# Optimization experiments

Hardware: AMD Instinct MI355X
Metric: run time of the kernel (lower is better)

The kernel has to match this reference:

```python
import jax, jax.numpy as jnp
import numpy as np

EMBED = 1024
HEADS = 16
HEAD_DIM = EMBED // HEADS


def setup_inputs() -> dict:
    key = jax.random.key(0)
    ks = jax.random.split(key, 11)
    B, S, E = 4, 2048, EMBED
    scale = 1.0 / np.sqrt(E)
    inp = {
        "Q": jax.random.normal(ks[0], (B, S, E), jnp.float32),
        "K": jax.random.normal(ks[1], (B, S, E), jnp.float32),
        "V": jax.random.normal(ks[2], (B, S, E), jnp.float32),
        "Wq": jax.random.normal(ks[3], (E, E), jnp.float32) * scale,
        "Wk": jax.random.normal(ks[4], (E, E), jnp.float32) * scale,
        "Wv": jax.random.normal(ks[5], (E, E), jnp.float32) * scale,
        "Wo": jax.random.normal(ks[6], (E, E), jnp.float32) * scale,
        "bq": jax.random.normal(ks[7], (E,), jnp.float32) * 0.01,
        "bk": jax.random.normal(ks[8], (E,), jnp.float32) * 0.01,
        "bv": jax.random.normal(ks[9], (E,), jnp.float32) * 0.01,
        "bo": jax.random.normal(ks[10], (E,), jnp.float32) * 0.01,
    }
    return inp


def reference(Q, K, V, Wq, Wk, Wv, Wo, bq, bk, bv, bo):
    B, S, E = Q.shape
    H, Dh = HEADS, HEAD_DIM
    # linear projections (torch Linear: x @ W.T + b)
    q = (Q @ Wq.T + bq).reshape(B, S, H, Dh).transpose(0, 2, 1, 3)  # [B,H,S,Dh]
    k = (K @ Wk.T + bk).reshape(B, S, H, Dh).transpose(0, 2, 1, 3)
    v = (V @ Wv.T + bv).reshape(B, S, H, Dh).transpose(0, 2, 1, 3)
    # scores [B,H,S,S]
    A = jnp.einsum('bhqd,bhkd->bhqk', q, k) / np.sqrt(Dh).astype(np.float32)
    # causal mask (mask=True)
    causal = jnp.tril(jnp.ones((S, S), dtype=bool))
    A = jnp.where(causal, A, -jnp.inf)
    w = jax.nn.softmax(A, axis=-1)
    out = jnp.einsum('bhqk,bhkd->bhqd', w, v)  # [B,H,S,Dh]
    out = out.transpose(0, 2, 1, 3).reshape(B, S, E)
    return out @ Wo.T + bo
```

## Files before the change

### kernel.cpp

```cpp
#include <hip/hip_runtime.h>
#include <hip/hip_bf16.h>
#include <hip/hip_fp16.h>

#define E_DIM 1024
#define N_HEADS 16
#define DH 64
#define BATCH 4
#define SEQ 2048
#define MROWS (BATCH * SEQ)
#define NQT 16

using half8 = __attribute__((ext_vector_type(8))) _Float16;
using half4v = __attribute__((ext_vector_type(4))) _Float16;
using fp16x2 = __attribute__((ext_vector_type(2))) __fp16;
using f32x4 = __attribute__((ext_vector_type(4))) float;

#define LOG2E 1.44269504088896340736f

__device__ inline half8 ld8(const _Float16* p) { return *(const half8*)p; }

__device__ inline uint32_t lds_off(const void* p) {
    return (uint32_t)(uintptr_t)(const __attribute__((address_space(3))) char*)p;
}

__device__ inline float exp2fast(float x) {
    float r;
    asm("v_exp_f32 %0, %1" : "=v"(r) : "v"(x));
    return r;
}

__global__ void cast3_f16(const float* __restrict__ a0, const float* __restrict__ a1,
                          const float* __restrict__ a2,
                          _Float16* __restrict__ o0, _Float16* __restrict__ o1,
                          _Float16* __restrict__ o2, int n4) {
    const int z = blockIdx.y;
    const float* in = z == 0 ? a0 : z == 1 ? a1 : a2;
    _Float16* out = z == 0 ? o0 : z == 1 ? o1 : o2;
    int i = blockIdx.x * blockDim.x + threadIdx.x;
    if (i < n4) {
        float4 v = *(const float4*)(in + (size_t)i * 4);
        half4v o;
        o[0] = (_Float16)v.x; o[1] = (_Float16)v.y;
        o[2] = (_Float16)v.z; o[3] = (_Float16)v.w;
        *(half4v*)(out + (size_t)i * 4) = o;
    }
}
__global__ void cast4_f16(const float* __restrict__ a0, const float* __restrict__ a1,
                          const float* __restrict__ a2, const float* __restrict__ a3,
                          _Float16* __restrict__ o0, _Float16* __restrict__ o1,
                          _Float16* __restrict__ o2, _Float16* __restrict__ o3, int n4) {
    const int z = blockIdx.y;
    const float* in = z == 0 ? a0 : z == 1 ? a1 : z == 2 ? a2 : a3;
    _Float16* out = z == 0 ? o0 : z == 1 ? o1 : z == 2 ? o2 : o3;
    int i = blockIdx.x * blockDim.x + threadIdx.x;
    if (i < n4) {
        float4 v = *(const float4*)(in + (size_t)i * 4);
        half4v o;
        o[0] = (_Float16)v.x; o[1] = (_Float16)v.y;
        o[2] = (_Float16)v.z; o[3] = (_Float16)v.w;
        *(half4v*)(out + (size_t)i * 4) = o;
    }
}

template <int MODE>
__device__ __forceinline__ void gemm_body(
    const _Float16* __restrict__ A, const _Float16* __restrict__ Bt,
    const float* __restrict__ bias, void* __restrict__ outp,
    int N, int K, float scale, _Float16* As, _Float16* Bs)
{
    const int t = threadIdx.x;
    const int w = t >> 6, l = t & 63;
    const int wr = w >> 1, wc = w & 1;
    const int lr = l & 15, lg = l >> 4;
    const long row0 = (long)blockIdx.x * 128;
    const long col0 = (long)blockIdx.y * 128;
    f32x4 acc[4][4] = {};

    for (int k0 = 0; k0 < K; k0 += 32) {
        __syncthreads();
        #pragma unroll
        for (int p = 0; p < 2; ++p) {
            const int n = p * 256 + t;
            const int row = n >> 2, c8 = (n & 3) << 3;
            const _Float16* ga = &A[(size_t)(row0 + row) * K + k0 + c8];
            const _Float16* gb = &Bt[(size_t)(col0 + row) * K + k0 + c8];
            __builtin_amdgcn_global_load_lds(
                (const __attribute__((address_space(1))) unsigned int*)ga,
                (__attribute__((address_space(3))) unsigned int*)((char*)As + n * 16), 16, 0, 0);
            __builtin_amdgcn_global_load_lds(
                (const __attribute__((address_space(1))) unsigned int*)gb,
                (__attribute__((address_space(3))) unsigned int*)((char*)Bs + n * 16), 16, 0, 0);
        }
        __syncthreads();
        half8 af[4], bf[4];
        #pragma unroll
        for (int i = 0; i < 4; i++) {
            af[i] = *(const half8*)&As[(wr * 64 + i * 16 + lr) * 32 + lg * 8];
            bf[i] = *(const half8*)&Bs[(wc * 64 + i * 16 + lr) * 32 + lg * 8];
        }
        #pragma unroll
        for (int i = 0; i < 4; i++)
            #pragma unroll
            for (int j = 0; j < 4; j++)
                acc[i][j] = __builtin_amdgcn_mfma_f32_16x16x32_f16(af[i], bf[j], acc[i][j], 0, 0, 0);
    }

    #pragma unroll
    for (int i = 0; i < 4; i++)
        #pragma unroll
        for (int j = 0; j < 4; j++)
            #pragma unroll
            for (int r = 0; r < 4; r++) {
                long row = row0 + wr * 64 + i * 16 + lg * 4 + r;
                long col = col0 + wc * 64 + j * 16 + lr;
                float v = acc[i][j][r] + bias[col];
                if (MODE == 0) {
                    ((float*)outp)[row * N + col] = v;
                } else {
                    long b = row >> 11, s = row & 2047;
                    long h = col >> 6, d = col & 63;
                    ((_Float16*)outp)[(((b * N_HEADS + h) * SEQ + s) << 6) + d] =
                        (_Float16)(v * scale);
                }
            }
}

__global__ __launch_bounds__(256) void gemm_qkv(
    const _Float16* __restrict__ A0, const _Float16* __restrict__ A1,
    const _Float16* __restrict__ A2,
    const _Float16* __restrict__ W0, const _Float16* __restrict__ W1,
    const _Float16* __restrict__ W2,
    const float* __restrict__ b0, const float* __restrict__ b1,
    const float* __restrict__ b2,
    _Float16* __restrict__ o0, _Float16* __restrict__ o1, _Float16* __restrict__ o2)
{
    __shared__ _Float16 As[128 * 32];
    __shared__ _Float16 Bs[128 * 32];
    const int z = blockIdx.z;
    const _Float16* A = z == 0 ? A0 : z == 1 ? A1 : A2;
    const _Float16* W = z == 0 ? W0 : z == 1 ? W1 : W2;
    const float* bia = z == 0 ? b0 : z == 1 ? b1 : b2;
    _Float16* o = z == 0 ? o0 : z == 1 ? o1 : o2;
    const float scale = z == 0 ? (0.125f * LOG2E) : 1.0f;
    gemm_body<1>(A, W, bia, o, E_DIM, E_DIM, scale, As, Bs);
}

__global__ __launch_bounds__(256) void gemm_out(
    const _Float16* __restrict__ A, const _Float16* __restrict__ W,
    const float* __restrict__ bias, float* __restrict__ o)
{
    __shared__ _Float16 As[128 * 32];
    __shared__ _Float16 Bs[128 * 32];
    gemm_body<0>(A, W, bias, o, E_DIM, E_DIM, 1.0f, As, Bs);
}

__global__ __launch_bounds__(256) void attn_fwd(
    const _Float16* __restrict__ qb, const _Float16* __restrict__ kb,
    const _Float16* __restrict__ vb, _Float16* __restrict__ ob)
{
    __shared__ _Float16 sB[3 * 8192];
    const int bh = blockIdx.x;
    const int tile = (NQT - 1) - blockIdx.y;
    const int t = threadIdx.x;
    const int w = t >> 6, l = t & 63;
    const int lr = l & 15, lg = l >> 4;
    const _Float16* qh = qb + (size_t)bh * SEQ * DH;
    const char* khc = (const char*)(kb + (size_t)bh * SEQ * DH);
    const char* vhc = (const char*)(vb + (size_t)bh * SEQ * DH);
    char* sBc = (char*)sB;
    const uint32_t ldsbase = lds_off(sB);
    const int b = bh >> 4, h = bh & 15;

    int koff[2], voff[2];
    #pragma unroll
    for (int i = 0; i < 2; ++i) {
        const int s = i * 256 + t;
        { const int r = s >> 3, c = (s & 7) ^ (r & 7);
          koff[i] = r * 128 + c * 16; }
        { const int r = ((s >> 5) << 2) | ((s >> 1) & 3);
          const int c = (((s >> 3) & 3) << 1) | (s & 1);
          voff[i] = r * 128 + c * 16; }
    }

    const int nt = 2 * tile + 2;
    const int q0 = tile * 128 + w * 16;
    const int q1 = q0 + 64;

    half8 qf00 = ld8(&qh[(q0 + lr) * DH + lg * 8]);
    half8 qf01 = ld8(&qh[(q0 + lr) * DH + 32 + lg * 8]);
    half8 qf10 = ld8(&qh[(q1 + lr) * DH + lg * 8]);
    half8 qf11 = ld8(&qh[(q1 + lr) * DH + 32 + lg * 8]);

    #define STAGE(TI, BUF) do {                                                   \
        const char* ks_ = khc + (size_t)(TI) * 8192;                              \
        const char* vs_ = vhc + (size_t)(TI) * 8192;                              \
        char* kd_ = sBc + (BUF) * 16384;                                          \
        char* vd_ = kd_ + 8192;                                                   \
        _Pragma("unroll")                                                         \
        for (int i_ = 0; i_ < 2; ++i_) {                                          \
            __builtin_amdgcn_global_load_lds(                                     \
                (const __attribute__((address_space(1))) unsigned int*)(ks_ + koff[i_]), \
                (__attribute__((address_space(3))) unsigned int*)(kd_ + i_ * 4096 + t * 16), 16, 0, 0); \
            __builtin_amdgcn_global_load_lds(                                     \
                (const __attribute__((address_space(1))) unsigned int*)(vs_ + voff[i_]), \
                (__attribute__((address_space(3))) unsigned int*)(vd_ + i_ * 4096 + t * 16), 16, 0, 0); \
        }                                                                         \
    } while (0)

    STAGE(0, 0);
    STAGE(1, 1);

    f32x4 acc0[4] = {}, acc1[4] = {};
    float m0 = -1e30f, l0 = 0.f, m1 = -1e30f, l1 = 0.f;

    int cur = 0;
    #pragma unroll 1
    for (int it = 0; it < nt; ++it) {
        if (it + 1 < nt) asm volatile("s_waitcnt vmcnt(4)" ::: "memory");
        else             asm volatile("s_waitcnt vmcnt(0)" ::: "memory");
        __builtin_amdgcn_s_barrier();
        if (it + 2 < nt) {
            int nb = cur + 2; if (nb >= 3) nb -= 3;
            STAGE(it + 2, nb);
        }

        const char* kbuf = sBc + cur * 16384;
        const uint32_t vbuf = ldsbase + (uint32_t)cur * 16384u + 8192u;
        const bool a0 = (it <= 2 * tile);
        const bool diag0 = (it == 2 * tile);
        const bool diag1 = (it == 2 * tile + 1);

        f32x4 st0[4], st1[4];
        __builtin_amdgcn_s_setprio(1);
        #pragma unroll
        for (int sub = 0; sub < 4; ++sub) {
            const int row = sub * 16 + lr;
            half8 kf0 = *(const half8*)(kbuf + ((row * 128 + lg * 16) ^ ((row & 7) << 4)));
            half8 kf1 = *(const half8*)(kbuf + ((row * 128 + 64 + lg * 16) ^ ((row & 7) << 4)));
            f32x4 s1 = {};
            s1 = __builtin_amdgcn_mfma_f32_16x16x32_f16(kf0, qf10, s1, 0, 0, 0);
            s1 = __builtin_amdgcn_mfma_f32_16x16x32_f16(kf1, qf11, s1, 0, 0, 0);
            st1[sub] = s1;
            if (a0) {
                f32x4 s0 = {};
                s0 = __builtin_amdgcn_mfma_f32_16x16x32_f16(kf0, qf00, s0, 0, 0, 0);
                s0 = __builtin_amdgcn_mfma_f32_16x16x32_f16(kf1, qf01, s0, 0, 0, 0);
                st0[sub] = s0;
            }
        }
        __builtin_amdgcn_s_setprio(0);

        half4v pa0[4], pa1[4];

        if (a0) {
            if (diag0) {
                #pragma unroll
                for (int sub = 0; sub < 4; ++sub)
                    #pragma unroll
                    for (int r = 0; r < 4; ++r)
                        if (sub * 16 + lg * 4 + r > w * 16 + lr) st0[sub][r] = -1e30f;
            }
            float a = fmaxf(fmaxf(st0[0][0], st0[0][1]), st0[0][2]);
            float bb = fmaxf(fmaxf(st0[0][3], st0[1][0]), st0[1][1]);
            float c = fmaxf(fmaxf(st0[1][2], st0[1][3]), st0[2][0]);
            float d = fmaxf(fmaxf(st0[2][1], st0[2][2]), st0[2][3]);
            float e = fmaxf(fmaxf(st0[3][0], st0[3][1]), st0[3][2]);
            float tmax = fmaxf(fmaxf(fmaxf(a, bb), fmaxf(c, d)), fmaxf(e, st0[3][3]));
            tmax = fmaxf(tmax, __shfl_xor(tmax, 16, 64));
            tmax = fmaxf(tmax, __shfl_xor(tmax, 32, 64));
            const bool skip = __all(tmax <= m0 + 10.0f);
            float fscale = 1.0f;
            if (!skip) { const float mn = fmaxf(m0, tmax); fscale = exp2fast(m0 - mn); m0 = mn; }
            float psum = 0.f;
            fp16x2 ones; ones[0] = (__fp16)1.f; ones[1] = (__fp16)1.f;
            #pragma unroll
            for (int sub = 0; sub < 4; ++sub) {
                float pv[4];
                #pragma unroll
                for (int r = 0; r < 4; ++r) pv[r] = exp2fast(st0[sub][r] - m0);
                fp16x2 lo = __builtin_amdgcn_cvt_pkrtz(pv[0], pv[1]);
                fp16x2 hi = __builtin_amdgcn_cvt_pkrtz(pv[2], pv[3]);
                psum = __builtin_amdgcn_fdot2(lo, ones, psum, false);
                psum = __builtin_amdgcn_fdot2(hi, ones, psum, false);
                pa0[sub][0] = (_Float16)lo[0]; pa0[sub][1] = (_Float16)lo[1];
                pa0[sub][2] = (_Float16)hi[0]; pa0[sub][3] = (_Float16)hi[1];
            }
            l0 = l0 * fscale + psum;
            if (!skip) {
                #pragma unroll
                for (int r = 0; r < 4; ++r) {
                    const float fr = __shfl(fscale, lg * 4 + r, 64);
                    acc0[0][r] *= fr; acc0[1][r] *= fr; acc0[2][r] *= fr; acc0[3][r] *= fr;
                }
            }
        }

        {
            if (diag1) {
                #pragma unroll
                for (int sub = 0; sub < 4; ++sub)
                    #pragma unroll
                    for (int r = 0; r < 4; ++r)
                        if (sub * 16 + lg * 4 + r > w * 16 + lr) st1[sub][r] = -1e30f;
            }
            float a = fmaxf(fmaxf(st1[0][0], st1[0][1]), st1[0][2]);
            float bb = fmaxf(fmaxf(st1[0][3], st1[1][0]), st1[1][1]);
            float c = fmaxf(fmaxf(st1[1][2], st1[1][3]), st1[2][0]);
            float d = fmaxf(fmaxf(st1[2][1], st1[2][2]), st1[2][3]);
            float e = fmaxf(fmaxf(st1[3][0], st1[3][1]), st1[3][2]);
            float tmax = fmaxf(fmaxf(fmaxf(a, bb), fmaxf(c, d)), fmaxf(e, st1[3][3]));
            tmax = fmaxf(tmax, __shfl_xor(tmax, 16, 64));
            tmax = fmaxf(tmax, __shfl_xor(tmax, 32, 64));
            const bool skip = __all(tmax <= m1 + 10.0f);
            float fscale = 1.0f;
            if (!skip) { const float mn = fmaxf(m1, tmax); fscale = exp2fast(m1 - mn); m1 = mn; }
            float psum = 0.f;
            fp16x2 ones; ones[0] = (__fp16)1.f; ones[1] = (__fp16)1.f;
            #pragma unroll
            for (int sub = 0; sub < 4; ++sub) {
                float pv[4];
                #pragma unroll
                for (int r = 0; r < 4; ++r) pv[r] = exp2fast(st1[sub][r] - m1);
                fp16x2 lo = __builtin_amdgcn_cvt_pkrtz(pv[0], pv[1]);
                fp16x2 hi = __builtin_amdgcn_cvt_pkrtz(pv[2], pv[3]);
                psum = __builtin_amdgcn_fdot2(lo, ones, psum, false);
                psum = __builtin_amdgcn_fdot2(hi, ones, psum, false);
                pa1[sub][0] = (_Float16)lo[0]; pa1[sub][1] = (_Float16)lo[1];
                pa1[sub][2] = (_Float16)hi[0]; pa1[sub][3] = (_Float16)hi[1];
            }
            l1 = l1 * fscale + psum;
            if (!skip) {
                #pragma unroll
                for (int r = 0; r < 4; ++r) {
                    const float fr = __shfl(fscale, lg * 4 + r, 64);
                    acc1[0][r] *= fr; acc1[1][r] *= fr; acc1[2][r] *= fr; acc1[3][r] *= fr;
                }
            }
        }

        __builtin_amdgcn_s_setprio(1);
        #pragma unroll
        for (int sub = 0; sub < 4; ++sub) {
            const uint32_t a0addr = vbuf + (uint32_t)((sub * 4 + lg) * 512 + lr * 8);
            half4v vf0, vf1, vf2, vf3;
            asm volatile("ds_read_b64_tr_b16 %0, %1" : "=v"(vf0) : "v"(a0addr));
            asm volatile("ds_read_b64_tr_b16 %0, %1 offset:128" : "=v"(vf1) : "v"(a0addr));
            asm volatile("ds_read_b64_tr_b16 %0, %1 offset:256" : "=v"(vf2) : "v"(a0addr));
            asm volatile("ds_read_b64_tr_b16 %0, %1 offset:384" : "=v"(vf3) : "v"(a0addr));
            asm volatile("s_waitcnt lgkmcnt(0)");
            __builtin_amdgcn_sched_barrier(0);
            acc1[0] = __builtin_amdgcn_mfma_f32_16x16x16f16(pa1[sub], vf0, acc1[0], 0, 0, 0);
            acc1[1] = __builtin_amdgcn_mfma_f32_16x16x16f16(pa1[sub], vf1, acc1[1], 0, 0, 0);
            acc1[2] = __builtin_amdgcn_mfma_f32_16x16x16f16(pa1[sub], vf2, acc1[2], 0, 0, 0);
            acc1[3] = __builtin_amdgcn_mfma_f32_16x16x16f16(pa1[sub], vf3, acc1[3], 0, 0, 0);
            if (a0) {
                acc0[0] = __builtin_amdgcn_mfma_f32_16x16x16f16(pa0[sub], vf0, acc0[0], 0, 0, 0);
                acc0[1] = __builtin_amdgcn_mfma_f32_16x16x16f16(pa0[sub], vf1, acc0[1], 0, 0, 0);
                acc0[2] = __builtin_amdgcn_mfma_f32_16x16x16f16(pa0[sub], vf2, acc0[2], 0, 0, 0);
                acc0[3] = __builtin_amdgcn_mfma_f32_16x16x16f16(pa0[sub], vf3, acc0[3], 0, 0, 0);
            }
        }
        __builtin_amdgcn_s_setprio(0);

        cur = (cur + 1 == 3) ? 0 : cur + 1;
    }
    #undef STAGE

    l0 += __shfl_xor(l0, 16, 64); l0 += __shfl_xor(l0, 32, 64);
    l1 += __shfl_xor(l1, 16, 64); l1 += __shfl_xor(l1, 32, 64);
    const float inv0 = 1.f / l0, inv1 = 1.f / l1;
    #pragma unroll
    for (int r = 0; r < 4; ++r) {
        const float ir0 = __shfl(inv0, lg * 4 + r, 64);
        const float ir1 = __shfl(inv1, lg * 4 + r, 64);
        const int qr0 = q0 + lg * 4 + r;
        const int qr1 = q1 + lg * 4 + r;
        #pragma unroll
        for (int db = 0; db < 4; ++db) {
            ob[((size_t)(b * SEQ + qr0)) * E_DIM + h * DH + db * 16 + lr] =
                (_Float16)(acc0[db][r] * ir0);
            ob[((size_t)(b * SEQ + qr1)) * E_DIM + h * DH + db * 16 + lr] =
                (_Float16)(acc1[db][r] * ir1);
        }
    }
}

extern "C" void kernel_launch(void* const* d_in, const int* in_sizes, int n_in,
                              void* d_out, int out_size, void* d_ws, size_t ws_size,
                              hipStream_t stream) {
    const float* Q  = (const float*)d_in[0];
    const float* K  = (const float*)d_in[1];
    const float* V  = (const float*)d_in[2];
    const float* Wq = (const float*)d_in[3];
    const float* Wk = (const float*)d_in[4];
    const float* Wv = (const float*)d_in[5];
    const float* Wo = (const float*)d_in[6];
    const float* bq = (const float*)d_in[7];
    const float* bk = (const float*)d_in[8];
    const float* bv = (const float*)d_in[9];
    const float* bo = (const float*)d_in[10];

    const size_t NX = (size_t)MROWS * E_DIM;
    const size_t NW = (size_t)E_DIM * E_DIM;

    _Float16* ws  = (_Float16*)d_ws;
    _Float16* Xq  = ws;
    _Float16* Xk  = Xq + NX;
    _Float16* Xv  = Xk + NX;
    _Float16* hWq = Xv + NX;
    _Float16* hWk = hWq + NW;
    _Float16* hWv = hWk + NW;
    _Float16* hWo = hWv + NW;
    _Float16* qbf = hWo + NW;
    _Float16* kbf = qbf + NX;
    _Float16* vbf = kbf + NX;
    _Float16* aof = vbf + NX;

    const int n4x = (int)(NX / 4), n4w = (int)(NW / 4);
    cast3_f16<<<dim3((n4x + 255) / 256, 3), 256, 0, stream>>>(Q, K, V, Xq, Xk, Xv, n4x);
    cast4_f16<<<dim3((n4w + 255) / 256, 4), 256, 0, stream>>>(Wq, Wk, Wv, Wo, hWq, hWk, hWv, hWo, n4w);

    dim3 gg3(MROWS / 128, E_DIM / 128, 3);
    gemm_qkv<<<gg3, 256, 0, stream>>>(Xq, Xk, Xv, hWq, hWk, hWv, bq, bk, bv, qbf, kbf, vbf);

    attn_fwd<<<dim3(BATCH * N_HEADS, NQT), 256, 0, stream>>>(qbf, kbf, vbf, aof);

    dim3 gg(MROWS / 128, E_DIM / 128);
    gemm_out<<<gg, 256, 0, stream>>>(aof, hWo, bo, (float*)d_out);
}
```

Before: 200.0 us.

## Fuse fp32-to-fp16 activation cast into QKV GEMM and double-buffer attention

Removes the separate cast kernel for Q/K/V activations. The QKV GEMM now loads fp32 tiles straight into LDS with an XOR swizzle and converts them to fp16 in registers before the MFMA, saving a full write and re-read of three large fp16 buffers. The attention kernel also drops from a 3-stage to a 2-stage K/V ring buffer and issues the next prefetch after an extra barrier at the end of each iteration. This lowers LDS use but exposes more load latency. The GEMM now moves twice as many A-tile bytes per K step and adds conversion work in the inner loop.

```diff
diff --git a/kernel.cpp b/kernel.cpp
--- a/kernel.cpp
+++ b/kernel.cpp
@@ -29,22 +29,11 @@
     return r;
 }
 
-__global__ void cast3_f16(const float* __restrict__ a0, const float* __restrict__ a1,
-                          const float* __restrict__ a2,
-                          _Float16* __restrict__ o0, _Float16* __restrict__ o1,
-                          _Float16* __restrict__ o2, int n4) {
-    const int z = blockIdx.y;
-    const float* in = z == 0 ? a0 : z == 1 ? a1 : a2;
-    _Float16* out = z == 0 ? o0 : z == 1 ? o1 : o2;
-    int i = blockIdx.x * blockDim.x + threadIdx.x;
-    if (i < n4) {
-        float4 v = *(const float4*)(in + (size_t)i * 4);
-        half4v o;
-        o[0] = (_Float16)v.x; o[1] = (_Float16)v.y;
-        o[2] = (_Float16)v.z; o[3] = (_Float16)v.w;
-        *(half4v*)(out + (size_t)i * 4) = o;
-    }
-}
+#define GLOAD_LDS(SRC, DST) \
+    __builtin_amdgcn_global_load_lds( \
+        (const __attribute__((address_space(1))) unsigned int*)(SRC), \
+        (__attribute__((address_space(3))) unsigned int*)(DST), 16, 0, 0)
+
 __global__ void cast4_f16(const float* __restrict__ a0, const float* __restrict__ a1,
                           const float* __restrict__ a2, const float* __restrict__ a3,
                           _Float16* __restrict__ o0, _Float16* __restrict__ o1,
@@ -62,11 +51,11 @@
     }
 }
 
-template <int MODE>
+template <int MODE, int AF32>
 __device__ __forceinline__ void gemm_body(
-    const _Float16* __restrict__ A, const _Float16* __restrict__ Bt,
+    const void* __restrict__ Avoid, const _Float16* __restrict__ Bt,
     const float* __restrict__ bias, void* __restrict__ outp,
-    int N, int K, float scale, _Float16* As, _Float16* Bs)
+    int N, int K, float scale, char* As, _Float16* Bs)
 {
     const int t = threadIdx.x;
     const int w = t >> 6, l = t & 63;
@@ -78,24 +67,48 @@
 
     for (int k0 = 0; k0 < K; k0 += 32) {
         __syncthreads();
-        #pragma unroll
-        for (int p = 0; p < 2; ++p) {
-            const int n = p * 256 + t;
-            const int row = n >> 2, c8 = (n & 3) << 3;
-            const _Float16* ga = &A[(size_t)(row0 + row) * K + k0 + c8];
-            const _Float16* gb = &Bt[(size_t)(col0 + row) * K + k0 + c8];
-            __builtin_amdgcn_global_load_lds(
-                (const __attribute__((address_space(1))) unsigned int*)ga,
-                (__attribute__((address_space(3))) unsigned int*)((char*)As + n * 16), 16, 0, 0);
-            __builtin_amdgcn_global_load_lds(
-                (const __attribute__((address_space(1))) unsigned int*)gb,
-                (__attribute__((address_space(3))) unsigned int*)((char*)Bs + n * 16), 16, 0, 0);
+        if (AF32) {
+            const float* A = (const float*)Avoid;
+            #pragma unroll
+            for (int i = 0; i < 4; ++i) {
+                const int s = i * 256 + t;
+                const int row = s >> 3, c16 = (s & 7) ^ (row & 7);
+                GLOAD_LDS(&A[(size_t)(row0 + row) * K + k0 + c16 * 4], As + s * 16);
+            }
+            #pragma unroll
+            for (int p = 0; p < 2; ++p) {
+                const int n = p * 256 + t;
+                const int row = n >> 2, c8 = (n & 3) << 3;
+                GLOAD_LDS(&Bt[(size_t)(col0 + row) * K + k0 + c8], (char*)Bs + n * 16);
+            }
+        } else {
+            const _Float16* A = (const _Float16*)Avoid;
+            #pragma unroll
+            for (int p = 0; p < 2; ++p) {
+                const int n = p * 256 + t;
+                const int row = n >> 2, c8 = (n & 3) << 3;
+                GLOAD_LDS(&A[(size_t)(row0 + row) * K + k0 + c8], As + n * 16);
+                GLOAD_LDS(&Bt[(size_t)(col0 + row) * K + k0 + c8], (char*)Bs + n * 16);
+            }
         }
         __syncthreads();
         half8 af[4], bf[4];
         #pragma unroll
         for (int i = 0; i < 4; i++) {
-            af[i] = *(const half8*)&As[(wr * 64 + i * 16 + lr) * 32 + lg * 8];
+            const int row = wr * 64 + i * 16 + lr;
+            if (AF32) {
+                const int xr = (row & 7) << 4;
+                f32x4 lo = *(const f32x4*)(As + ((row * 128 + lg * 32) ^ xr));
+                f32x4 hi = *(const f32x4*)(As + ((row * 128 + lg * 32 + 16) ^ xr));
+                union { fp16x2 h2[4]; half8 h8; } u;
+                u.h2[0] = __builtin_amdgcn_cvt_pkrtz(lo[0], lo[1]);
+                u.h2[1] = __builtin_amdgcn_cvt_pkrtz(lo[2], lo[3]);
+                u.h2[2] = __builtin_amdgcn_cvt_pkrtz(hi[0], hi[1]);
+                u.h2[3] = __builtin_amdgcn_cvt_pkrtz(hi[2], hi[3]);
+                af[i] = u.h8;
+            } else {
+                af[i] = *(const half8*)&((const _Float16*)As)[row * 32 + lg * 8];
+            }
             bf[i] = *(const half8*)&Bs[(wc * 64 + i * 16 + lr) * 32 + lg * 8];
         }
         #pragma unroll
@@ -126,39 +139,39 @@
 }
 
 __global__ __launch_bounds__(256) void gemm_qkv(
-    const _Float16* __restrict__ A0, const _Float16* __restrict__ A1,
-    const _Float16* __restrict__ A2,
+    const float* __restrict__ A0, const float* __restrict__ A1,
+    const float* __restrict__ A2,
     const _Float16* __restrict__ W0, const _Float16* __restrict__ W1,
     const _Float16* __restrict__ W2,
     const float* __restrict__ b0, const float* __restrict__ b1,
     const float* __restrict__ b2,
     _Float16* __restrict__ o0, _Float16* __restrict__ o1, _Float16* __restrict__ o2)
 {
-    __shared__ _Float16 As[128 * 32];
+    __shared__ char As[128 * 32 * 4];
     __shared__ _Float16 Bs[128 * 32];
     const int z = blockIdx.z;
-    const _Float16* A = z == 0 ? A0 : z == 1 ? A1 : A2;
+    const float* A = z == 0 ? A0 : z == 1 ? A1 : A2;
     const _Float16* W = z == 0 ? W0 : z == 1 ? W1 : W2;
     const float* bia = z == 0 ? b0 : z == 1 ? b1 : b2;
     _Float16* o = z == 0 ? o0 : z == 1 ? o1 : o2;
     const float scale = z == 0 ? (0.125f * LOG2E) : 1.0f;
-    gemm_body<1>(A, W, bia, o, E_DIM, E_DIM, scale, As, Bs);
+    gemm_body<1, 1>(A, W, bia, o, E_DIM, E_DIM, scale, As, Bs);
 }
 
 __global__ __launch_bounds__(256) void gemm_out(
     const _Float16* __restrict__ A, const _Float16* __restrict__ W,
     const float* __restrict__ bias, float* __restrict__ o)
 {
-    __shared__ _Float16 As[128 * 32];
+    __shared__ char As[128 * 32 * 2];
     __shared__ _Float16 Bs[128 * 32];
-    gemm_body<0>(A, W, bias, o, E_DIM, E_DIM, 1.0f, As, Bs);
+    gemm_body<0, 0>(A, W, bias, o, E_DIM, E_DIM, 1.0f, As, Bs);
 }
 
 __global__ __launch_bounds__(256) void attn_fwd(
     const _Float16* __restrict__ qb, const _Float16* __restrict__ kb,
     const _Float16* __restrict__ vb, _Float16* __restrict__ ob)
 {
-    __shared__ _Float16 sB[3 * 8192];
+    __shared__ _Float16 sB[2 * 8192];
     const int bh = blockIdx.x;
     const int tile = (NQT - 1) - blockIdx.y;
     const int t = threadIdx.x;
@@ -198,12 +211,8 @@
         char* vd_ = kd_ + 8192;                                                   \
         _Pragma("unroll")                                                         \
         for (int i_ = 0; i_ < 2; ++i_) {                                          \
-            __builtin_amdgcn_global_load_lds(                                     \
-                (const __attribute__((address_space(1))) unsigned int*)(ks_ + koff[i_]), \
-                (__attribute__((address_space(3))) unsigned int*)(kd_ + i_ * 4096 + t * 16), 16, 0, 0); \
-            __builtin_amdgcn_global_load_lds(                                     \
-                (const __attribute__((address_space(1))) unsigned int*)(vs_ + voff[i_]), \
-                (__attribute__((address_space(3))) unsigned int*)(vd_ + i_ * 4096 + t * 16), 16, 0, 0); \
+            GLOAD_LDS(ks_ + koff[i_], kd_ + i_ * 4096 + t * 16);                  \
+            GLOAD_LDS(vs_ + voff[i_], vd_ + i_ * 4096 + t * 16);                  \
         }                                                                         \
     } while (0)
 
@@ -219,10 +228,6 @@
         if (it + 1 < nt) asm volatile("s_waitcnt vmcnt(4)" ::: "memory");
         else             asm volatile("s_waitcnt vmcnt(0)" ::: "memory");
         __builtin_amdgcn_s_barrier();
-        if (it + 2 < nt) {
-            int nb = cur + 2; if (nb >= 3) nb -= 3;
-            STAGE(it + 2, nb);
-        }
 
         const char* kbuf = sBc + cur * 16384;
         const uint32_t vbuf = ldsbase + (uint32_t)cur * 16384u + 8192u;
@@ -362,7 +367,9 @@
         }
         __builtin_amdgcn_s_setprio(0);
 
-        cur = (cur + 1 == 3) ? 0 : cur + 1;
+        __builtin_amdgcn_s_barrier();
+        if (it + 2 < nt) STAGE(it + 2, cur);
+        cur ^= 1;
     }
     #undef STAGE
 
@@ -404,10 +411,7 @@
     const size_t NW = (size_t)E_DIM * E_DIM;
 
     _Float16* ws  = (_Float16*)d_ws;
-    _Float16* Xq  = ws;
-    _Float16* Xk  = Xq + NX;
-    _Float16* Xv  = Xk + NX;
-    _Float16* hWq = Xv + NX;
+    _Float16* hWq = ws;
     _Float16* hWk = hWq + NW;
     _Float16* hWv = hWk + NW;
     _Float16* hWo = hWv + NW;
@@ -416,12 +420,11 @@
     _Float16* vbf = kbf + NX;
     _Float16* aof = vbf + NX;
 
-    const int n4x = (int)(NX / 4), n4w = (int)(NW / 4);
-    cast3_f16<<<dim3((n4x + 255) / 256, 3), 256, 0, stream>>>(Q, K, V, Xq, Xk, Xv, n4x);
+    const int n4w = (int)(NW / 4);
     cast4_f16<<<dim3((n4w + 255) / 256, 4), 256, 0, stream>>>(Wq, Wk, Wv, Wo, hWq, hWk, hWv, hWo, n4w);
 
     dim3 gg3(MROWS / 128, E_DIM / 128, 3);
-    gemm_qkv<<<gg3, 256, 0, stream>>>(Xq, Xk, Xv, hWq, hWk, hWv, bq, bk, bv, qbf, kbf, vbf);
+    gemm_qkv<<<gg3, 256, 0, stream>>>(Q, K, V, hWq, hWk, hWv, bq, bk, bv, qbf, kbf, vbf);
 
     attn_fwd<<<dim3(BATCH * N_HEADS, NQT), 256, 0, stream>>>(qbf, kbf, vbf, aof);
 
```

After: 184.7 us. -7.6%, faster.
